# Kernel optimization log

Hardware: AMD Instinct MI355X
Metric: run time of the kernel (lower is better)

Reference implementation:

```python
import jax, jax.numpy as jnp
import numpy as np

RADIUS2 = 0.03 ** 2
SIM_THRESH = 0.7
EPS = 1e-8


def setup_inputs() -> dict:
    key = jax.random.key(0)
    k1, k2, k3, k4, k5, k6, k7 = jax.random.split(key, 7)
    B, N, D = 2, 6144, 32
    # points in a 0.3-side cube so radius 0.03 gives realistic neighbor counts
    points = jax.random.uniform(k1, (B, N, 3), dtype=jnp.float32) * 0.3
    embeddings = jax.random.normal(k2, (B, N, D), dtype=jnp.float32)
    leaf_mask = jax.random.randint(k3, (B, N), 0, 2, dtype=jnp.int32)
    # consistency_net: Linear(2D, D) -> ReLU -> Linear(D, D)
    W1 = jax.random.normal(k4, (2 * D, D), dtype=jnp.float32) * (1.0 / np.sqrt(2 * D))
    b1 = jax.random.normal(k5, (D,), dtype=jnp.float32) * 0.01
    W2 = jax.random.normal(k6, (D, D), dtype=jnp.float32) * (1.0 / np.sqrt(D))
    b2 = jax.random.normal(k7, (D,), dtype=jnp.float32) * 0.01
    return {"points": points, "embeddings": embeddings, "leaf_mask": leaf_mask,
            "W1": W1, "b1": b1, "W2": W2, "b2": b2}


def reference(points, embeddings, leaf_mask, W1, b1, W2, b2):
    # points: [B,N,3], embeddings: [B,N,D], leaf_mask: [B,N] int (0/1)
    dt = embeddings.dtype
    leaf = leaf_mask > 0  # [B,N] bool

    # pairwise squared distances via the Gram trick (avoids [B,N,N,3])
    pn = jnp.sum(points * points, axis=-1)                      # [B,N]
    gram = jnp.einsum('bic,bjc->bij', points, points)           # [B,N,N]
    d2 = jnp.maximum(pn[:, :, None] + pn[:, None, :] - 2.0 * gram, 0.0)

    # neighbor mask: within radius AND neighbor is leaf (matches dist<0.03 & leaf_mask)
    nb = (d2 < RADIUS2) & leaf[:, None, :]                      # [B,N,N]

    # cosine similarity with torch's eps clamp on norms
    enorm = jnp.maximum(jnp.linalg.norm(embeddings, axis=-1), EPS)  # [B,N]
    inner = jnp.einsum('bid,bjd->bij', embeddings, embeddings)      # [B,N,N]
    sims = inner / (enorm[:, :, None] * enorm[:, None, :])

    sim_mask = nb & (sims > SIM_THRESH)                          # [B,N,N]
    cnt_nb = jnp.sum(nb, axis=-1)                                # [B,N]
    cnt_sim = jnp.sum(sim_mask, axis=-1)                         # [B,N]

    # mean of similar-neighbor embeddings
    sum_sim = jnp.einsum('bij,bjd->bid', sim_mask.astype(dt), embeddings)
    mean_sim = sum_sim / jnp.maximum(cnt_sim, 1).astype(dt)[..., None]

    # consistency MLP on [center_embedding, mean_similar]
    combined = jnp.concatenate([embeddings, mean_sim], axis=-1)  # [B,N,2D]
    h = jax.nn.relu(jnp.einsum('bnk,kd->bnd', combined, W1) + b1)
    out = jnp.einsum('bnk,kd->bnd', h, W2) + b2                  # [B,N,D]

    # refine only leaf points with >1 neighbor and >0 similar neighbors
    cond = leaf & (cnt_nb > 1) & (cnt_sim > 0)                   # [B,N]
    refined = jnp.where(cond[..., None], out, embeddings)

    # per-batch early exit: sum(leaf_mask) < 10 -> unchanged
    batch_ok = jnp.sum(leaf_mask, axis=-1) >= 10                 # [B]
    return jnp.where(batch_ok[:, None, None], refined, embeddings)
```

## Files before the change

kernel.cpp:

```cpp
#include <hip/hip_runtime.h>

#define NPTS    6144
#define DIM     32
#define NB      2
#define NCELL   1000
#define R2      0.0009f
#define NWAVES  4
#define BLOCK   (NWAVES * 64)
#define LEAFBIT 8192
#define PPT     6
#define NBCAP   128

__device__ __forceinline__ int cellof(float x) {
    int c = (int)(x * (10.0f / 0.3f));
    return min(max(c, 0), 9);
}

#define WS_LEAF   0
#define WS_CSTART 4
#define WS_SORTED 2008

__global__ __launch_bounds__(1024)
void build_cells(const float* __restrict__ points, const int* __restrict__ leaf,
                 int* __restrict__ ws)
{
    __shared__ int s_hist[1024];
    __shared__ int s_cursor[1024];
    __shared__ int s_wsum[16];
    __shared__ int s_leaf;

    const int t = threadIdx.x;
    const int b = blockIdx.x;
    const int w = t >> 6, lane = t & 63;

    s_hist[t] = 0;
    if (t == 0) s_leaf = 0;

    float px[PPT], py[PPT], pz[PPT];
    int   pc[PPT], pw[PPT];

    __syncthreads();

    int lc = 0;
    #pragma unroll
    for (int r = 0; r < PPT; ++r) {
        const int i  = r * 1024 + t;
        const int gi = b * NPTS + i;
        px[r] = points[gi * 3 + 0];
        py[r] = points[gi * 3 + 1];
        pz[r] = points[gi * 3 + 2];
        const int lf = leaf[gi] > 0 ? 1 : 0;
        lc += lf;
        pc[r] = (cellof(pz[r]) * 10 + cellof(py[r])) * 10 + cellof(px[r]);
        pw[r] = i + (lf ? LEAFBIT : 0);
        atomicAdd(&s_hist[pc[r]], 1);
    }
    #pragma unroll
    for (int off = 32; off > 0; off >>= 1) lc += __shfl_down(lc, off);
    if (lane == 0) atomicAdd(&s_leaf, lc);
    __syncthreads();

    const int v = s_hist[t];
    int x = v;
    #pragma unroll
    for (int off = 1; off < 64; off <<= 1) {
        const int y = __shfl_up(x, off);
        if (lane >= off) x += y;
    }
    if (lane == 63) s_wsum[w] = x;
    __syncthreads();
    if (t < 16) {
        int wv = s_wsum[t];
        #pragma unroll
        for (int off = 1; off < 16; off <<= 1) {
            const int y = __shfl_up(wv, off);
            if (t >= off) wv += y;
        }
        s_wsum[t] = wv;
    }
    __syncthreads();
    const int incl = x + (w > 0 ? s_wsum[w - 1] : 0);
    s_cursor[t] = incl - v;

    if (t < NCELL) ws[WS_CSTART + b * (NCELL + 1) + t + 1] = incl;
    if (t == 0) {
        ws[WS_CSTART + b * (NCELL + 1)] = 0;
        ws[WS_LEAF + b] = s_leaf;
    }
    __syncthreads();

    float4* sorted = (float4*)(ws + WS_SORTED) + (size_t)b * NPTS;
    #pragma unroll
    for (int r = 0; r < PPT; ++r) {
        const int pos = atomicAdd(&s_cursor[pc[r]], 1);
        sorted[pos] = make_float4(px[r], py[r], pz[r], (float)pw[r]);
    }
}

__global__ __launch_bounds__(BLOCK)
void refine(const float* __restrict__ emb,
            const float* __restrict__ W1, const float* __restrict__ b1,
            const float* __restrict__ W2, const float* __restrict__ b2,
            const int* __restrict__ ws, float* __restrict__ out)
{
    __shared__ __align__(16) float s_ei[NWAVES][DIM];
    __shared__ float s_mean[NWAVES][DIM];
    __shared__ float s_h[NWAVES][DIM];
    __shared__ int   s_nb[NWAVES][NBCAP];
    __shared__ int   s_sv[NWAVES][NBCAP];
    __shared__ __align__(16) float s_W1[2 * DIM * DIM];
    __shared__ __align__(16) float s_W2[DIM * DIM];
    __shared__ float s_b1[DIM], s_b2[DIM];

    const int tid  = threadIdx.x;
    const int wid  = tid >> 6;
    const int lane = tid & 63;
    const int s    = blockIdx.x * NWAVES + wid;
    const int b    = s / NPTS;
    const int slot = s - b * NPTS;

    const float4* srt  = (const float4*)(ws + WS_SORTED) + (size_t)b * NPTS;
    const int*    cst  = ws + WS_CSTART + b * (NCELL + 1);
    const float*  embB = emb + (size_t)b * NPTS * DIM;

    {
        const float4* w1v = (const float4*)W1;
        float4*       sw1 = (float4*)s_W1;
        for (int idx = tid; idx < (2 * DIM * DIM) / 4; idx += BLOCK) sw1[idx] = w1v[idx];
        const float4* w2v = (const float4*)W2;
        float4*       sw2 = (float4*)s_W2;
        for (int idx = tid; idx < (DIM * DIM) / 4; idx += BLOCK) sw2[idx] = w2v[idx];
        if (tid < DIM) { s_b1[tid] = b1[tid]; s_b2[tid] = b2[tid]; }
    }

    const float4 P  = srt[slot];
    const int    iw = (int)P.w;
    const int    io = iw & (LEAFBIT - 1);
    const bool   li = (iw & LEAFBIT) != 0;
    const bool   ok = ws[WS_LEAF + b] >= 10;

    if (lane < DIM) s_ei[wid][lane] = embB[(size_t)io * DIM + lane];

    __syncthreads();

    float ni2 = 0.0f;
    #pragma unroll
    for (int d = 0; d < DIM; ++d) { const float v = s_ei[wid][d]; ni2 += v * v; }
    const float rni = 1.0f / fmaxf(sqrtf(ni2), 1e-8f);

    const int cx = cellof(P.x), cy = cellof(P.y), cz = cellof(P.z);

    int begv = 0, lenv = 0;
    if (lane < 9) {
        const int z = cz + lane / 3 - 1;
        const int y = cy + lane % 3 - 1;
        if ((unsigned)z <= 9u && (unsigned)y <= 9u) {
            const int rowb = (z * 10 + y) * 10;
            const int c0   = rowb + max(cx - 1, 0);
            const int c1   = rowb + min(cx + 1, 9);
            begv = cst[c0];
            lenv = cst[c1 + 1] - begv;
        }
    }
    const int rb0 = __shfl(begv, 0), rb1 = __shfl(begv, 1), rb2 = __shfl(begv, 2);
    const int rb3 = __shfl(begv, 3), rb4 = __shfl(begv, 4), rb5 = __shfl(begv, 5);
    const int rb6 = __shfl(begv, 6), rb7 = __shfl(begv, 7), rb8 = __shfl(begv, 8);
    const int ln0 = __shfl(lenv, 0), ln1 = __shfl(lenv, 1), ln2 = __shfl(lenv, 2);
    const int ln3 = __shfl(lenv, 3), ln4 = __shfl(lenv, 4), ln5 = __shfl(lenv, 5);
    const int ln6 = __shfl(lenv, 6), ln7 = __shfl(lenv, 7), ln8 = __shfl(lenv, 8);
    const int pf1 = ln0,       pf2 = pf1 + ln1, pf3 = pf2 + ln2;
    const int pf4 = pf3 + ln3, pf5 = pf4 + ln4, pf6 = pf5 + ln5;
    const int pf7 = pf6 + ln6, pf8 = pf7 + ln7, pf9 = pf8 + ln8;

    int nbcnt = 0;
    for (int base = 0; base < pf9; base += 64) {
        const int g = base + lane;
        int j = 0;
        if (g < pf9) j = rb8 + g - pf8;
        if (g < pf8) j = rb7 + g - pf7;
        if (g < pf7) j = rb6 + g - pf6;
        if (g < pf6) j = rb5 + g - pf5;
        if (g < pf5) j = rb4 + g - pf4;
        if (g < pf4) j = rb3 + g - pf3;
        if (g < pf3) j = rb2 + g - pf2;
        if (g < pf2) j = rb1 + g - pf1;
        if (g < pf1) j = rb0 + g;
        const float4 Q  = srt[j];
        const float dx = Q.x - P.x, dy = Q.y - P.y, dz = Q.z - P.z;
        const float d2 = dx * dx + dy * dy + dz * dz;
        const int   jw = (int)Q.w;
        const bool  nb = (g < pf9) && (d2 < R2) && ((jw & LEAFBIT) != 0);
        const unsigned long long m = __ballot(nb);
        if (nb) {
            const int pos = nbcnt + __popcll(m & ((1ull << lane) - 1ull));
            if (pos < NBCAP) s_nb[wid][pos] = jw & (LEAFBIT - 1);
        }
        nbcnt += __popcll(m);
    }
    const int cnt_nb = nbcnt;

    int csim = 0;
    const int nh = min(cnt_nb, NBCAP);
    for (int h0 = 0; h0 < nh; h0 += 64) {
        const int h = h0 + lane;
        bool surv = false;
        int  jo   = 0;
        if (h < nh) {
            jo = s_nb[wid][h];
            const float4* ej4 = (const float4*)(embB + (size_t)jo * DIM);
            float dot = 0.0f, nj2 = 0.0f;
            #pragma unroll
            for (int k = 0; k < DIM / 4; ++k) {
                const float4 v = ej4[k];
                const float4 a = *(const float4*)&s_ei[wid][4 * k];
                dot += a.x * v.x + a.y * v.y + a.z * v.z + a.w * v.w;
                nj2 += v.x * v.x + v.y * v.y + v.z * v.z + v.w * v.w;
            }
            const float rnj = 1.0f / fmaxf(sqrtf(nj2), 1e-8f);
            surv = (dot * rni * rnj) > 0.7f;
        }
        const unsigned long long m = __ballot(surv);
        if (surv) {
            const int pos = csim + __popcll(m & ((1ull << lane) - 1ull));
            s_sv[wid][pos] = jo;
        }
        csim += __popcll(m);
    }

    if (lane < DIM) {
        float msum = 0.0f;
        for (int v = 0; v < csim; ++v)
            msum += embB[(size_t)s_sv[wid][v] * DIM + lane];
        s_mean[wid][lane] = (csim > 0) ? msum / (float)csim : 0.0f;
    }

    const bool cond = ok && li && (cnt_nb > 1) && (csim > 0);

    float* outp = out + ((size_t)b * NPTS + io) * DIM;
    if (lane < DIM) {
        if (!cond) {
            outp[lane] = s_ei[wid][lane];
        } else {
            float a0 = s_b1[lane], a1 = 0.0f;
            #pragma unroll
            for (int k = 0; k < DIM; k += 2) {
                a0 = fmaf(s_ei[wid][k],     s_W1[k * DIM + lane],       a0);
                a1 = fmaf(s_ei[wid][k + 1], s_W1[(k + 1) * DIM + lane], a1);
            }
            #pragma unroll
            for (int k = 0; k < DIM; k += 2) {
                a0 = fmaf(s_mean[wid][k],     s_W1[(DIM + k) * DIM + lane],     a0);
                a1 = fmaf(s_mean[wid][k + 1], s_W1[(DIM + k + 1) * DIM + lane], a1);
            }
            s_h[wid][lane] = fmaxf(a0 + a1, 0.0f);
            float c0 = s_b2[lane], c1 = 0.0f;
            #pragma unroll
            for (int k = 0; k < DIM; k += 2) {
                c0 = fmaf(s_h[wid][k],     s_W2[k * DIM + lane],       c0);
                c1 = fmaf(s_h[wid][k + 1], s_W2[(k + 1) * DIM + lane], c1);
            }
            outp[lane] = c0 + c1;
        }
    }
}

extern "C" void kernel_launch(void* const* d_in, const int* in_sizes, int n_in,
                              void* d_out, int out_size, void* d_ws, size_t ws_size,
                              hipStream_t stream) {
    const float* points = (const float*)d_in[0];
    const float* emb    = (const float*)d_in[1];
    const int*   leaf   = (const int*)d_in[2];
    const float* W1     = (const float*)d_in[3];
    const float* b1     = (const float*)d_in[4];
    const float* W2     = (const float*)d_in[5];
    const float* b2     = (const float*)d_in[6];
    float*       outp   = (float*)d_out;
    int*         ws     = (int*)d_ws;

    build_cells<<<NB, 1024, 0, stream>>>(points, leaf, ws);

    const int grid = (NB * NPTS) / NWAVES;
    refine<<<grid, BLOCK, 0, stream>>>(emb, W1, b1, W2, b2, ws, outp);
}
```

Before: 92.64 us.

## Drop shared weight staging and early-exit non-leaf points per wave

Stops staging W1/W2/b1/b2 into shared memory in every block and reads the weights directly from global memory (cached), which also removes the block-wide barrier. Waves whose point is non-leaf or whose batch fails the leaf-count check now copy the embedding with float4 stores and return before the neighbor search. The mean of similar neighbors is computed only when the refinement condition holds. This reduces LDS footprint and per-block setup, in exchange for weight loads going through the cache on each MLP evaluation.

Result: faster. 88.52 us (-4.4%).

```diff
diff --git a/kernel.cpp b/kernel.cpp
--- a/kernel.cpp
+++ b/kernel.cpp
@@ -108,9 +108,6 @@
     __shared__ float s_h[NWAVES][DIM];
     __shared__ int   s_nb[NWAVES][NBCAP];
     __shared__ int   s_sv[NWAVES][NBCAP];
-    __shared__ __align__(16) float s_W1[2 * DIM * DIM];
-    __shared__ __align__(16) float s_W2[DIM * DIM];
-    __shared__ float s_b1[DIM], s_b2[DIM];
 
     const int tid  = threadIdx.x;
     const int wid  = tid >> 6;
@@ -123,25 +120,21 @@
     const int*    cst  = ws + WS_CSTART + b * (NCELL + 1);
     const float*  embB = emb + (size_t)b * NPTS * DIM;
 
-    {
-        const float4* w1v = (const float4*)W1;
-        float4*       sw1 = (float4*)s_W1;
-        for (int idx = tid; idx < (2 * DIM * DIM) / 4; idx += BLOCK) sw1[idx] = w1v[idx];
-        const float4* w2v = (const float4*)W2;
-        float4*       sw2 = (float4*)s_W2;
-        for (int idx = tid; idx < (DIM * DIM) / 4; idx += BLOCK) sw2[idx] = w2v[idx];
-        if (tid < DIM) { s_b1[tid] = b1[tid]; s_b2[tid] = b2[tid]; }
-    }
-
     const float4 P  = srt[slot];
     const int    iw = (int)P.w;
     const int    io = iw & (LEAFBIT - 1);
     const bool   li = (iw & LEAFBIT) != 0;
     const bool   ok = ws[WS_LEAF + b] >= 10;
 
-    if (lane < DIM) s_ei[wid][lane] = embB[(size_t)io * DIM + lane];
-
-    __syncthreads();
+    const float4* e4   = (const float4*)(embB + (size_t)io * DIM);
+    float4*       out4 = (float4*)(out + ((size_t)b * NPTS + io) * DIM);
+
+    if (!(ok && li)) {
+        if (lane < DIM / 4) out4[lane] = e4[lane];
+        return;
+    }
+
+    if (lane < DIM) s_ei[wid][lane] = ((const float*)e4)[lane];
 
     float ni2 = 0.0f;
     #pragma unroll
@@ -227,39 +220,36 @@
         csim += __popcll(m);
     }
 
-    if (lane < DIM) {
-        float msum = 0.0f;
-        for (int v = 0; v < csim; ++v)
-            msum += embB[(size_t)s_sv[wid][v] * DIM + lane];
-        s_mean[wid][lane] = (csim > 0) ? msum / (float)csim : 0.0f;
-    }
-
-    const bool cond = ok && li && (cnt_nb > 1) && (csim > 0);
-
-    float* outp = out + ((size_t)b * NPTS + io) * DIM;
+    const bool cond = (cnt_nb > 1) && (csim > 0);
+
     if (lane < DIM) {
         if (!cond) {
-            outp[lane] = s_ei[wid][lane];
+            out[((size_t)b * NPTS + io) * DIM + lane] = s_ei[wid][lane];
         } else {
-            float a0 = s_b1[lane], a1 = 0.0f;
+            float msum = 0.0f;
+            for (int v = 0; v < csim; ++v)
+                msum += embB[(size_t)s_sv[wid][v] * DIM + lane];
+            s_mean[wid][lane] = msum / (float)csim;
+
+            float a0 = b1[lane], a1 = 0.0f;
             #pragma unroll
             for (int k = 0; k < DIM; k += 2) {
-                a0 = fmaf(s_ei[wid][k],     s_W1[k * DIM + lane],       a0);
-                a1 = fmaf(s_ei[wid][k + 1], s_W1[(k + 1) * DIM + lane], a1);
+                a0 = fmaf(s_ei[wid][k],     W1[k * DIM + lane],       a0);
+                a1 = fmaf(s_ei[wid][k + 1], W1[(k + 1) * DIM + lane], a1);
             }
             #pragma unroll
             for (int k = 0; k < DIM; k += 2) {
-                a0 = fmaf(s_mean[wid][k],     s_W1[(DIM + k) * DIM + lane],     a0);
-                a1 = fmaf(s_mean[wid][k + 1], s_W1[(DIM + k + 1) * DIM + lane], a1);
+                a0 = fmaf(s_mean[wid][k],     W1[(DIM + k) * DIM + lane],     a0);
+                a1 = fmaf(s_mean[wid][k + 1], W1[(DIM + k + 1) * DIM + lane], a1);
             }
             s_h[wid][lane] = fmaxf(a0 + a1, 0.0f);
-            float c0 = s_b2[lane], c1 = 0.0f;
+            float c0 = b2[lane], c1 = 0.0f;
             #pragma unroll
             for (int k = 0; k < DIM; k += 2) {
-                c0 = fmaf(s_h[wid][k],     s_W2[k * DIM + lane],       c0);
-                c1 = fmaf(s_h[wid][k + 1], s_W2[(k + 1) * DIM + lane], c1);
-            }
-            outp[lane] = c0 + c1;
+                c0 = fmaf(s_h[wid][k],     W2[k * DIM + lane],       c0);
+                c1 = fmaf(s_h[wid][k + 1], W2[(k + 1) * DIM + lane], c1);
+            }
+            out[((size_t)b * NPTS + io) * DIM + lane] = c0 + c1;
         }
     }
 }
```
